# Kernel tuning notes

Measured on AMD Instinct MI355X. Metric: run time of the kernel, lower is better.

Reference implementation:

```python
import jax, jax.numpy as jnp
import numpy as np

D_MODEL = 256
D_FFN = 1024
N_HEADS = 8
N_LEVELS = 4
N_POINTS = 4
SPATIAL = np.array([[60, 100], [30, 50], [15, 25], [8, 13]], dtype=np.int32)  # (H, W) per level


def _layer_norm(x, g, b, eps=1e-5):
    mu = jnp.mean(x, axis=-1, keepdims=True)
    var = jnp.mean(jnp.square(x - mu), axis=-1, keepdims=True)
    return (x - mu) * jax.lax.rsqrt(var + eps) * g + b


def _bilinear_sample(v_l, loc, aw, H, W):
    # v_l: (B,H,W,h,hd); loc: (B,Lq,h,p,2) normalized [0,1]; aw: (B,Lq,h,p)
    B = v_l.shape[0]
    h = v_l.shape[3]
    x = loc[..., 0] * W - 0.5  # grid_sample align_corners=False convention
    y = loc[..., 1] * H - 0.5
    x0 = jnp.floor(x)
    y0 = jnp.floor(y)
    lx = x - x0
    ly = y - y0
    x0i = x0.astype(jnp.int32)
    y0i = y0.astype(jnp.int32)
    bi = jnp.arange(B)[:, None, None, None]
    hi = jnp.arange(h)[None, None, :, None]

    def g(xi, yi):
        valid = (xi >= 0) & (xi < W) & (yi >= 0) & (yi < H)
        xc = jnp.clip(xi, 0, W - 1)
        yc = jnp.clip(yi, 0, H - 1)
        return v_l[bi, yc, xc, hi] * valid[..., None].astype(v_l.dtype)  # zero padding

    w00 = (1 - lx) * (1 - ly)
    w01 = lx * (1 - ly)
    w10 = (1 - lx) * ly
    w11 = lx * ly
    samp = (g(x0i, y0i) * w00[..., None] + g(x0i + 1, y0i) * w01[..., None]
            + g(x0i, y0i + 1) * w10[..., None] + g(x0i + 1, y0i + 1) * w11[..., None])
    # weighted sum over sampling points -> (B,Lq,h,hd)
    return jnp.einsum('blhpd,blhp->blhd', samp, aw)


def _msda(q, val, ref, W_value, b_value, W_off, b_off, W_attn, b_attn, W_out, b_out):
    # mmcv MultiScaleDeformableAttention (batch_first, identity=query, eval-mode dropout)
    B, Lq, C = q.shape
    hd = C // N_HEADS
    v = (val @ W_value + b_value).reshape(B, -1, N_HEADS, hd)
    off = (q @ W_off + b_off).reshape(B, Lq, N_HEADS, N_LEVELS, N_POINTS, 2)
    aw = jax.nn.softmax((q @ W_attn + b_attn).reshape(B, Lq, N_HEADS, N_LEVELS * N_POINTS), axis=-1)
    aw = aw.reshape(B, Lq, N_HEADS, N_LEVELS, N_POINTS)
    normalizer = jnp.asarray(SPATIAL[:, ::-1].copy(), dtype=q.dtype)  # (levels, 2) = (W, H)
    loc = ref[:, :, None, :, None, :] + off / normalizer[None, None, None, :, None, :]
    out = jnp.zeros((B, Lq, N_HEADS, hd), q.dtype)
    start = 0
    for lvl in range(N_LEVELS):
        H, W = int(SPATIAL[lvl, 0]), int(SPATIAL[lvl, 1])
        v_l = v[:, start:start + H * W].reshape(B, H, W, N_HEADS, hd)
        start += H * W
        out = out + _bilinear_sample(v_l, loc[:, :, :, lvl], aw[:, :, :, lvl], H, W)
    return q + out.reshape(B, Lq, C) @ W_out + b_out  # identity + output_proj


def setup_inputs() -> dict:
    key = jax.random.key(0)
    ks = jax.random.split(key, 16)
    bs, cams, nq = 1, 6, 6400
    l = int(SPATIAL.prod(axis=1).sum())
    s = 0.02
    inp = {
        'query': jax.random.normal(ks[0], (bs, nq, D_MODEL), jnp.float32),
        'key': jax.random.normal(ks[1], (bs, cams, l, D_MODEL), jnp.float32),
        'value': jax.random.normal(ks[2], (bs, cams, l, D_MODEL), jnp.float32),
        'reference_points_cam': jax.random.uniform(ks[3], (cams, bs, nq, N_LEVELS, 2), jnp.float32),
        'spatial_shapes': jnp.asarray(SPATIAL),
        'level_start_index': jnp.asarray(np.concatenate([[0], np.cumsum(SPATIAL.prod(axis=1))[:-1]]).astype(np.int32)),
        'bev_mask': jax.random.randint(ks[4], (cams, bs, nq, 4), 0, 2).astype(jnp.int32),
        'W_value': jax.random.normal(ks[5], (D_MODEL, D_MODEL), jnp.float32) * s,
        'b_value': jnp.zeros((D_MODEL,), jnp.float32),
        'W_off': jax.random.normal(ks[6], (D_MODEL, N_HEADS * N_LEVELS * N_POINTS * 2), jnp.float32) * s,
        'b_off': jax.random.normal(ks[7], (N_HEADS * N_LEVELS * N_POINTS * 2,), jnp.float32) * s,
        'W_attn': jax.random.normal(ks[8], (D_MODEL, N_HEADS * N_LEVELS * N_POINTS), jnp.float32) * s,
        'b_attn': jnp.zeros((N_HEADS * N_LEVELS * N_POINTS,), jnp.float32),
        'W_out': jax.random.normal(ks[9], (D_MODEL, D_MODEL), jnp.float32) * s,
        'b_out': jnp.zeros((D_MODEL,), jnp.float32),
        'ln1_g': jnp.ones((D_MODEL,), jnp.float32),
        'ln1_b': jnp.zeros((D_MODEL,), jnp.float32),
        'W1': jax.random.normal(ks[10], (D_MODEL, D_FFN), jnp.float32) * s,
        'b1': jnp.zeros((D_FFN,), jnp.float32),
        'W2': jax.random.normal(ks[11], (D_FFN, D_MODEL), jnp.float32) * s,
        'b2': jnp.zeros((D_MODEL,), jnp.float32),
        'ln2_g': jnp.ones((D_MODEL,), jnp.float32),
        'ln2_b': jnp.zeros((D_MODEL,), jnp.float32),
    }
    return inp


def reference(query, key, value, reference_points_cam, spatial_shapes, level_start_index, bev_mask,
              W_value, b_value, W_off, b_off, W_attn, b_attn, W_out, b_out,
              ln1_g, ln1_b, W1, b1, W2, b2, ln2_g, ln2_b):
    bs, nq, C = query.shape
    cams = key.shape[1]
    l = key.shape[2]
    # per-camera query visibility taken from batch element 0 (as in original)
    cam_mask = (bev_mask[:, 0].sum(-1) > 0).astype(query.dtype)  # (cams, nq)
    # rebatch via masking: equivalent to gather-to-padded since attention is per-query
    q_rb = (query[:, None] * cam_mask[None, :, :, None]).reshape(bs * cams, nq, C)
    ref_rb = (jnp.transpose(reference_points_cam, (1, 0, 2, 3, 4))
              * cam_mask[None, :, :, None, None]).reshape(bs * cams, nq, N_LEVELS, 2)
    val = value.reshape(bs * cams, l, C)
    attn = _msda(q_rb, val, ref_rb, W_value, b_value, W_off, b_off, W_attn, b_attn, W_out, b_out)
    attn = attn.reshape(bs, cams, nq, C)
    # scatter-add back (only visible camera contributions)
    slots = jnp.einsum('bknc,kn->bnc', attn, cam_mask)
    # visibility count (full bev_mask, per batch element)
    count = (bev_mask.sum(-1) > 0).astype(query.dtype)  # (cams, bs, nq)
    count = jnp.maximum(count.transpose(1, 2, 0).sum(-1), 1.0)  # (bs, nq)
    slots = slots / count[..., None]
    x = _layer_norm(slots + query, ln1_g, ln1_b)
    ffn = jax.nn.relu(x @ W1 + b1) @ W2 + b2
    return _layer_norm(x + ffn, ln2_g, ln2_b)
```

## Files before the change

kernel.cpp:

```cpp
#include <hip/hip_runtime.h>
#include <math.h>

#define NQ      6400
#define NCAMS   6
#define LTOT    7979
#define DM      256
#define DFFN    1024

typedef __attribute__((ext_vector_type(8))) short bf16x8;
typedef __attribute__((ext_vector_type(4))) float f32x4;
typedef __attribute__((ext_vector_type(2))) float f32x2;

__device__ inline unsigned short f32_to_bf16(float f) {
    unsigned u = __float_as_uint(f);
    unsigned r = u + 0x7FFF + ((u >> 16) & 1);
    return (unsigned short)(r >> 16);
}

__device__ inline unsigned cvt_pk_bf16(float lo, float hi) {
    unsigned r;
    asm("v_cvt_pk_bf16_f32 %0, %1, %2" : "=v"(r) : "v"(lo), "v"(hi));
    return r;
}
__device__ inline unsigned short cvt1_bf16(float x) {
    return (unsigned short)cvt_pk_bf16(x, 0.f);
}

__global__ __launch_bounds__(256) void wt_head_kernel(
    const float* __restrict__ Wv, const float* __restrict__ Woff,
    const float* __restrict__ Wattn, unsigned short* __restrict__ wsT)
{
    int b = blockIdx.x;
    const float* src; int K, N, t0, dstoff;
    if (b < 64)       { src = Wv;    K = 256; N = 256; t0 = 0;   dstoff = 0; }
    else if (b < 128) { src = Woff;  K = 256; N = 256; t0 = 64;  dstoff = 65536; }
    else              { src = Wattn; K = 256; N = 128; t0 = 128; dstoff = 131072; }
    int t = b - t0;
    int ntn = N >> 5;
    int kt = t / ntn, nt = t - kt * ntn;
    __shared__ float tile[32][33];
    int tx = threadIdx.x & 31, ty = threadIdx.x >> 5;
    #pragma unroll
    for (int i = 0; i < 4; ++i)
        tile[ty + i * 8][tx] = src[(size_t)(kt * 32 + ty + i * 8) * N + nt * 32 + tx];
    __syncthreads();
    #pragma unroll
    for (int i = 0; i < 4; ++i) {
        int nn = nt * 32 + ty + i * 8;
        wsT[dstoff + (size_t)nn * K + kt * 32 + tx] = f32_to_bf16(tile[tx][ty + i * 8]);
    }
}

__global__ __launch_bounds__(256) void head_kernel(
    const float* __restrict__ value, const float* __restrict__ query,
    const unsigned short* __restrict__ WvT, const unsigned short* __restrict__ WqT,
    const float* __restrict__ bv, const float* __restrict__ boff,
    const float* __restrict__ battn,
    unsigned char* __restrict__ vb, unsigned short* __restrict__ qoffb,
    unsigned short* __restrict__ qawb)
{
    __shared__ __align__(16) unsigned char smem[20480];
    const int b = blockIdx.x;
    const int tid = threadIdx.x;
    const int wave = tid >> 6, lane = tid & 63;
    const int wm = wave >> 1, wn = wave & 1;
    const int quad = lane >> 4, l16 = lane & 15;

    if (b < 750) {
        unsigned short (*As)[40] = (unsigned short(*)[40])smem;
        unsigned short (*Bs)[40] = (unsigned short(*)[40])(smem + 10240);
        const int m0 = (b >> 1) * 128, n0 = (b & 1) * 128;
        const int M = NCAMS * LTOT;

        f32x4 acc[4][4] = {};

        for (int k0 = 0; k0 < 256; k0 += 32) {
            #pragma unroll
            for (int i = 0; i < 2; ++i) {
                int idx = tid + 256 * i;
                int r = idx >> 2, kc = (idx & 3) * 8;
                int gr = m0 + r;
                float4 f0, f1;
                if (gr < M) {
                    f0 = *(const float4*)(value + (size_t)gr * 256 + k0 + kc);
                    f1 = *(const float4*)(value + (size_t)gr * 256 + k0 + kc + 4);
                } else { f0 = make_float4(0.f,0.f,0.f,0.f); f1 = f0; }
                uint4 o;
                o.x = cvt_pk_bf16(f0.x, f0.y);
                o.y = cvt_pk_bf16(f0.z, f0.w);
                o.z = cvt_pk_bf16(f1.x, f1.y);
                o.w = cvt_pk_bf16(f1.z, f1.w);
                *(uint4*)&As[r][kc] = o;
            }
            #pragma unroll
            for (int i = 0; i < 2; ++i) {
                int idx = tid + 256 * i;
                int r = idx >> 2, kc = (idx & 3) * 8;
                *(uint4*)&Bs[r][kc] = *(const uint4*)(WvT + (size_t)(n0 + r) * 256 + k0 + kc);
            }
            __syncthreads();
            bf16x8 af[4], bfr[4];
            #pragma unroll
            for (int mi = 0; mi < 4; ++mi)
                af[mi] = *(const bf16x8*)&As[wm * 64 + mi * 16 + l16][quad * 8];
            #pragma unroll
            for (int ni = 0; ni < 4; ++ni)
                bfr[ni] = *(const bf16x8*)&Bs[wn * 64 + ni * 16 + l16][quad * 8];
            #pragma unroll
            for (int mi = 0; mi < 4; ++mi)
                #pragma unroll
                for (int ni = 0; ni < 4; ++ni)
                    acc[mi][ni] = __builtin_amdgcn_mfma_f32_16x16x32_bf16(
                        af[mi], bfr[ni], acc[mi][ni], 0, 0, 0);
            __syncthreads();
        }

        #pragma unroll
        for (int mi = 0; mi < 4; ++mi) {
            #pragma unroll
            for (int r = 0; r < 4; ++r) {
                int gm = m0 + wm * 64 + mi * 16 + quad * 4 + r;
                if (gm >= M) continue;
                int cam = gm / LTOT;
                int pix = gm - cam * LTOT;
                #pragma unroll
                for (int p = 0; p < 2; ++p) {
                    int gn0 = n0 + wn * 64 + p * 32 + l16;
                    int head = gn0 >> 5;
                    float v0 = acc[mi][2 * p][r]     + bv[gn0];
                    float v1 = acc[mi][2 * p + 1][r] + bv[gn0 + 16];
                    int pk = __builtin_amdgcn_cvt_pk_fp8_f32(v0, v1, 0, false);
                    *(unsigned short*)(vb + (((size_t)(cam * 8 + head)) * LTOT + pix) * 32
                                       + 2 * l16) = (unsigned short)pk;
                }
            }
        }
    } else {
        unsigned short (*As)[40] = (unsigned short(*)[40])smem;
        unsigned short (*Bs)[40] = (unsigned short(*)[40])(smem + 5120);
        const int t = b - 750;
        const int bx = t / 100, by = t % 100;
        const int m0 = by * 64, n0 = bx * 128;
        const int is_attn = (bx == 2);

        f32x4 acc[2][4] = {};

        for (int k0 = 0; k0 < 256; k0 += 32) {
            {
                int r = tid >> 2, kc = (tid & 3) * 8;
                float4 f0 = *(const float4*)(query + (size_t)(m0 + r) * 256 + k0 + kc);
                float4 f1 = *(const float4*)(query + (size_t)(m0 + r) * 256 + k0 + kc + 4);
                uint4 o;
                o.x = cvt_pk_bf16(f0.x, f0.y);
                o.y = cvt_pk_bf16(f0.z, f0.w);
                o.z = cvt_pk_bf16(f1.x, f1.y);
                o.w = cvt_pk_bf16(f1.z, f1.w);
                *(uint4*)&As[r][kc] = o;
            }
            #pragma unroll
            for (int i = 0; i < 2; ++i) {
                int idx = tid + 256 * i;
                int r = idx >> 2, kc = (idx & 3) * 8;
                *(uint4*)&Bs[r][kc] = *(const uint4*)(WqT + (size_t)(n0 + r) * 256 + k0 + kc);
            }
            __syncthreads();
            bf16x8 af[2], bfr[4];
            #pragma unroll
            for (int mi = 0; mi < 2; ++mi)
                af[mi] = *(const bf16x8*)&As[wm * 32 + mi * 16 + l16][quad * 8];
            #pragma unroll
            for (int ni = 0; ni < 4; ++ni)
                bfr[ni] = *(const bf16x8*)&Bs[wn * 64 + ni * 16 + l16][quad * 8];
            #pragma unroll
            for (int mi = 0; mi < 2; ++mi)
                #pragma unroll
                for (int ni = 0; ni < 4; ++ni)
                    acc[mi][ni] = __builtin_amdgcn_mfma_f32_16x16x32_bf16(
                        af[mi], bfr[ni], acc[mi][ni], 0, 0, 0);
            __syncthreads();
        }

        if (is_attn) {
            #pragma unroll
            for (int mi = 0; mi < 2; ++mi) {
                #pragma unroll
                for (int r = 0; r < 4; ++r) {
                    int gm = m0 + wm * 32 + mi * 16 + quad * 4 + r;
                    #pragma unroll
                    for (int ni = 0; ni < 4; ++ni) {
                        int gn = wn * 64 + ni * 16 + l16;
                        float v = acc[mi][ni][r] + battn[gn];
                        float mx = v;
                        #pragma unroll
                        for (int s = 1; s < 16; s <<= 1)
                            mx = fmaxf(mx, __shfl_xor(mx, s, 64));
                        float e = __expf(v - mx);
                        float sum = e;
                        #pragma unroll
                        for (int s = 1; s < 16; s <<= 1)
                            sum += __shfl_xor(sum, s, 64);
                        qawb[(size_t)gm * 128 + gn] = f32_to_bf16(e / sum);
                    }
                }
            }
        } else {
            #pragma unroll
            for (int mi = 0; mi < 2; ++mi) {
                #pragma unroll
                for (int r = 0; r < 4; ++r) {
                    int gm = m0 + wm * 32 + mi * 16 + quad * 4 + r;
                    #pragma unroll
                    for (int ni = 0; ni < 4; ++ni) {
                        int gn = n0 + wn * 64 + ni * 16 + l16;
                        qoffb[(size_t)gm * 256 + gn] = f32_to_bf16(acc[mi][ni][r] + boff[gn]);
                    }
                }
            }
        }
    }
}

__global__ __launch_bounds__(256) void sample_kernel(
    const unsigned char* __restrict__ vb,
    const unsigned short* __restrict__ qoffb,
    const unsigned short* __restrict__ qawb,
    const float* __restrict__ refpts,
    const int*   __restrict__ bev_mask,
    const float* __restrict__ Wout, const float* __restrict__ W1,
    const float* __restrict__ W2,
    unsigned short* __restrict__ outsum,
    float* __restrict__ visb,
    unsigned short* __restrict__ wsT)
{
    __shared__ __align__(16) unsigned s_tab[NCAMS][272][4];
    __shared__ float s_vis[NCAMS][16];
    __shared__ int   s_nvis[16];

    const int bid = blockIdx.x;
    const int tid = threadIdx.x;

    if (bid >= 3200) {
        int t = bid - 3200;
        const float* src; int K, N, dstoff;
        if (t < 64)       { src = Wout; K = 256;  N = 256;  dstoff = 163840; }
        else if (t < 320) { src = W1;   K = 256;  N = 1024; dstoff = 229376; t -= 64; }
        else              { src = W2;   K = 1024; N = 256;  dstoff = 491520; t -= 320; }
        int ntn = N >> 5;
        int kt = t / ntn, nt = t - kt * ntn;
        float (*tile)[33] = (float(*)[33])&s_tab[0][0][0];
        int tx = tid & 31, ty = tid >> 5;
        #pragma unroll
        for (int i = 0; i < 4; ++i)
            tile[ty + i * 8][tx] = src[(size_t)(kt * 32 + ty + i * 8) * N + nt * 32 + tx];
        __syncthreads();
        int txp = (dstoff == 163840) ? (((tx & 15) << 1) | (tx >> 4)) : tx;
        #pragma unroll
        for (int i = 0; i < 4; ++i) {
            int nn = nt * 32 + ty + i * 8;
            wsT[dstoff + (size_t)nn * K + kt * 32 + txp] = f32_to_bf16(tile[tx][ty + i * 8]);
        }
        return;
    }

    const int h   = bid & 7;
    const int q0  = (bid >> 3) * 16;
    const int sq  = tid >> 4;
    const int tup = tid & 15;
    const int lvl = tup >> 2;
    const int n_s = q0 + sq;

    if (tid < 96) {
        int cam = tid >> 4, q = tid & 15;
        const int* bm = bev_mask + ((size_t)cam * NQ + q0 + q) * 4;
        s_vis[cam][q] = ((bm[0] + bm[1] + bm[2] + bm[3]) > 0) ? 1.f : 0.f;
    }
    __syncthreads();
    if (tid >= 32 && tid < 48) {
        int q = tid - 32;
        float s = 0.f;
        #pragma unroll
        for (int cam = 0; cam < NCAMS; ++cam) s += s_vis[cam][q];
        s_nvis[q] = (int)s;
    }

    unsigned uoff = *(const unsigned*)(qoffb + (size_t)n_s * 256 + h * 32 + tup * 2);
    const float offx  = __uint_as_float(uoff << 16);
    const float offy  = __uint_as_float(uoff & 0xFFFF0000u);
    const float my_aw = __uint_as_float((unsigned)qawb[(size_t)n_s * 128 + h * 16 + tup] << 16);
    const int Wl   = (lvl == 0) ? 100 : (lvl == 1) ? 50 : (lvl == 2) ? 25 : 13;
    const int Hl   = (lvl == 0) ? 60  : (lvl == 1) ? 30 : (lvl == 2) ? 15 : 8;
    const int base = (lvl == 0) ? 0   : (lvl == 1) ? 6000 : (lvl == 2) ? 7500 : 7875;
    const float dx = offx / (float)Wl;
    const float dy = offy / (float)Hl;
    const int tabi = sq * 17 + tup;

    float2 rp[NCAMS];
    #pragma unroll
    for (int k = 0; k < NCAMS; ++k)
        rp[k] = *(const float2*)(refpts + (((size_t)k * NQ + n_s) * 4 + lvl) * 2);
    __syncthreads();

    #pragma unroll
    for (int k = 0; k < NCAMS; ++k) {
        float fx = (rp[k].x + dx) * (float)Wl - 0.5f;
        float fy = (rp[k].y + dy) * (float)Hl - 0.5f;
        float x0f = floorf(fx), y0f = floorf(fy);
        float lx = fx - x0f, ly = fy - y0f;
        int x0 = (int)x0f, y0 = (int)y0f;
        int x1 = x0 + 1, y1 = y0 + 1;
        float wb = my_aw * s_vis[k][sq];
        float w00 = (1.f - lx) * (1.f - ly) * wb;
        float w01 = lx * (1.f - ly) * wb;
        float w10 = (1.f - lx) * ly * wb;
        float w11 = lx * ly * wb;
        bool vx0 = (x0 >= 0) & (x0 < Wl), vx1 = (x1 >= 0) & (x1 < Wl);
        bool vy0 = (y0 >= 0) & (y0 < Hl), vy1 = (y1 >= 0) & (y1 < Hl);
        uint4 o;
        o.x = (vx0 & vy0) ? (((unsigned)(base + y0 * Wl + x0) << 16) | f32_to_bf16(w00)) : 0u;
        o.y = (vx1 & vy0) ? (((unsigned)(base + y0 * Wl + x1) << 16) | f32_to_bf16(w01)) : 0u;
        o.z = (vx0 & vy1) ? (((unsigned)(base + y1 * Wl + x0) << 16) | f32_to_bf16(w10)) : 0u;
        o.w = (vx1 & vy1) ? (((unsigned)(base + y1 * Wl + x1) << 16) | f32_to_bf16(w11)) : 0u;
        *(uint4*)&s_tab[k][tabi][0] = o;
    }
    __syncthreads();

    const int tp  = (tid >> 1) & 7;
    const int cg2 = tid & 1;

    f32x2 A[8] = {};

    #pragma unroll
    for (int k = 0; k < NCAMS; ++k) {
        const char* vkh = (const char*)vb + (size_t)(k * 8 + h) * (LTOT * 32) + cg2 * 16;
        #pragma unroll
        for (int t = 0; t < 2; ++t) {
            uint4 t4 = *(const uint4*)&s_tab[k][sq * 17 + tp * 2 + t][0];
            #pragma unroll
            for (int corner = 0; corner < 4; ++corner) {
                unsigned tc = (corner == 0) ? t4.x : (corner == 1) ? t4.y
                            : (corner == 2) ? t4.z : t4.w;
                float w = __uint_as_float(tc << 16);
                f32x2 w2 = {w, w};
                uint4 d = *(const uint4*)(vkh + ((size_t)(tc >> 16) << 5));
                A[0] += w2 * __builtin_amdgcn_cvt_pk_f32_fp8(d.x, false);
                A[1] += w2 * __builtin_amdgcn_cvt_pk_f32_fp8(d.x, true);
                A[2] += w2 * __builtin_amdgcn_cvt_pk_f32_fp8(d.y, false);
                A[3] += w2 * __builtin_amdgcn_cvt_pk_f32_fp8(d.y, true);
                A[4] += w2 * __builtin_amdgcn_cvt_pk_f32_fp8(d.z, false);
                A[5] += w2 * __builtin_amdgcn_cvt_pk_f32_fp8(d.z, true);
                A[6] += w2 * __builtin_amdgcn_cvt_pk_f32_fp8(d.w, false);
                A[7] += w2 * __builtin_amdgcn_cvt_pk_f32_fp8(d.w, true);
            }
        }
    }

    #pragma unroll
    for (int i = 0; i < 8; ++i) {
        float x0 = A[i].x, x1 = A[i].y;
        x0 += __shfl_xor(x0, 2, 64); x1 += __shfl_xor(x1, 2, 64);
        x0 += __shfl_xor(x0, 4, 64); x1 += __shfl_xor(x1, 4, 64);
        x0 += __shfl_xor(x0, 8, 64); x1 += __shfl_xor(x1, 8, 64);
        A[i].x = x0; A[i].y = x1;
    }

    if ((tid & 14) == 0) {
        int nv = s_nvis[sq];
        float sc = 1.f / (float)(nv > 0 ? nv : 1);
        uint4 o0, o1;
        o0.x = f32_to_bf16(A[0].x * sc) | ((unsigned)f32_to_bf16(A[0].y * sc) << 16);
        o0.y = f32_to_bf16(A[1].x * sc) | ((unsigned)f32_to_bf16(A[1].y * sc) << 16);
        o0.z = f32_to_bf16(A[2].x * sc) | ((unsigned)f32_to_bf16(A[2].y * sc) << 16);
        o0.w = f32_to_bf16(A[3].x * sc) | ((unsigned)f32_to_bf16(A[3].y * sc) << 16);
        o1.x = f32_to_bf16(A[4].x * sc) | ((unsigned)f32_to_bf16(A[4].y * sc) << 16);
        o1.y = f32_to_bf16(A[5].x * sc) | ((unsigned)f32_to_bf16(A[5].y * sc) << 16);
        o1.z = f32_to_bf16(A[6].x * sc) | ((unsigned)f32_to_bf16(A[6].y * sc) << 16);
        o1.w = f32_to_bf16(A[7].x * sc) | ((unsigned)f32_to_bf16(A[7].y * sc) << 16);
        *(uint4*)(outsum + (size_t)n_s * 256 + h * 32 + cg2 * 16)     = o0;
        *(uint4*)(outsum + (size_t)n_s * 256 + h * 32 + cg2 * 16 + 8) = o1;
    }
    if (h == 0 && tid < 16) visb[q0 + tid] = (s_nvis[tid] > 0) ? 1.f : 0.f;
}

__global__ __launch_bounds__(256) void tail_kernel(
    const unsigned short* __restrict__ A,
    const unsigned short* __restrict__ BT,
    const unsigned short* __restrict__ W1T,
    const unsigned short* __restrict__ W2T,
    const float* __restrict__ query, const float* __restrict__ visb,
    const float* __restrict__ b_out,
    const float* __restrict__ g1, const float* __restrict__ bln1,
    const float* __restrict__ fb1, const float* __restrict__ fb2,
    const float* __restrict__ g2, const float* __restrict__ bln2,
    float* __restrict__ out)
{
    __shared__ __align__(16) unsigned short As[32][40];
    __shared__ __align__(16) unsigned short Bs[256][40];
    __shared__ __align__(16) unsigned short Bs2[128][72];
    __shared__ __align__(16) unsigned short xs[32][264];
    __shared__ __align__(16) unsigned short hs[32][136];
    __shared__ float sred[2][4][4][2];
    __shared__ float ssred[2][4][4][2];
    __shared__ float s_mu[32], s_rs[32];

    const int tid  = threadIdx.x;
    const int wave = tid >> 6, lane = tid & 63;
    const int wm = wave >> 1, wn = wave & 1;
    const int quad = lane >> 4, l16 = lane & 15;
    const int m0 = blockIdx.x * 32;

    f32x4 acc[8] = {};

    for (int k0 = 0; k0 < 256; k0 += 32) {
        {
            int r = tid >> 3, kc = (tid & 7) * 4;
            *(uint2*)&As[r][kc] = *(const uint2*)(A + (size_t)(m0 + r) * 256 + k0 + kc);
        }
        {
            const unsigned short* src = BT + (size_t)tid * 256 + k0;
            *(uint4*)&Bs[tid][0]  = *(const uint4*)(src);
            *(uint4*)&Bs[tid][8]  = *(const uint4*)(src + 8);
            *(uint4*)&Bs[tid][16] = *(const uint4*)(src + 16);
            *(uint4*)&Bs[tid][24] = *(const uint4*)(src + 24);
        }
        __syncthreads();
        bf16x8 af = *(const bf16x8*)&As[wm * 16 + l16][quad * 8];
        #pragma unroll
        for (int ni = 0; ni < 8; ++ni) {
            bf16x8 bfr = *(const bf16x8*)&Bs[wn * 128 + ni * 16 + l16][quad * 8];
            acc[ni] = __builtin_amdgcn_mfma_f32_16x16x32_bf16(af, bfr, acc[ni], 0, 0, 0);
        }
        __syncthreads();
    }

    float vals[8][4];
    #pragma unroll
    for (int r = 0; r < 4; ++r) {
        int gm = m0 + wm * 16 + quad * 4 + r;
        float vs = visb[gm];
        float s = 0.f, ss = 0.f;
        #pragma unroll
        for (int ni = 0; ni < 8; ++ni) {
            int gn = wn * 128 + ni * 16 + l16;
            float v = acc[ni][r] + vs * b_out[gn]
                    + query[(size_t)gm * 256 + gn] * (1.f + vs);
            vals[ni][r] = v;
            s += v; ss += v * v;
        }
        #pragma unroll
        for (int m = 1; m < 16; m <<= 1) {
            s  += __shfl_xor(s,  m, 64);
            ss += __shfl_xor(ss, m, 64);
        }
        if (l16 == 0) {
            sred[wm][quad][r][wn]  = s;
            ssred[wm][quad][r][wn] = ss;
        }
    }
    __syncthreads();
    if (tid < 32) {
        int lwm = tid >> 4, lq = (tid >> 2) & 3, lr = tid & 3;
        float s  = sred[lwm][lq][lr][0]  + sred[lwm][lq][lr][1];
        float ss = ssred[lwm][lq][lr][0] + ssred[lwm][lq][lr][1];
        float mu = s * (1.f / 256.f);
        float var = ss * (1.f / 256.f) - mu * mu;
        s_mu[tid] = mu;
        s_rs[tid] = rsqrtf(var + 1e-5f);
    }
    __syncthreads();

    #pragma unroll
    for (int r = 0; r < 4; ++r) {
        int rowl = wm * 16 + quad * 4 + r;
        float mu = s_mu[rowl], rs = s_rs[rowl];
        #pragma unroll
        for (int ni = 0; ni < 8; ++ni) {
            int gn = wn * 128 + ni * 16 + l16;
            float res = (vals[ni][r] - mu) * rs * g1[gn] + bln1[gn];
            vals[ni][r] = res;
            xs[rowl][gn] = cvt1_bf16(res);
        }
    }

    f32x4 acc2[8] = {};

    for (int nc = 0; nc < 8; ++nc) {
        f32x4 hacc[4] = {};
        for (int k0 = 0; k0 < 256; k0 += 64) {
            #pragma unroll
            for (int i = 0; i < 4; ++i) {
                int idx = tid + 256 * i;
                int rr = idx >> 3, c8 = (idx & 7) * 8;
                *(uint4*)&Bs2[rr][c8] =
                    *(const uint4*)(W1T + (size_t)(nc * 128 + rr) * 256 + k0 + c8);
            }
            __syncthreads();
            #pragma unroll
            for (int s = 0; s < 2; ++s) {
                bf16x8 a2 = *(const bf16x8*)&xs[wm * 16 + l16][k0 + s * 32 + quad * 8];
                #pragma unroll
                for (int ni = 0; ni < 4; ++ni) {
                    bf16x8 b2v = *(const bf16x8*)&Bs2[wn * 64 + ni * 16 + l16][s * 32 + quad * 8];
                    hacc[ni] = __builtin_amdgcn_mfma_f32_16x16x32_bf16(a2, b2v, hacc[ni], 0, 0, 0);
                }
            }
            __syncthreads();
        }
        #pragma unroll
        for (int ni = 0; ni < 4; ++ni) {
            #pragma unroll
            for (int r = 0; r < 4; ++r) {
                int rowl = wm * 16 + quad * 4 + r;
                int col  = wn * 64 + ni * 16 + l16;
                hs[rowl][col] = cvt1_bf16(fmaxf(hacc[ni][r] + fb1[nc * 128 + col], 0.f));
            }
        }
        __syncthreads();
        #pragma unroll
        for (int ks = 0; ks < 4; ++ks) {
            {
                const unsigned short* src = W2T + (size_t)tid * 1024 + nc * 128 + ks * 32;
                *(uint4*)&Bs[tid][0]  = *(const uint4*)(src);
                *(uint4*)&Bs[tid][8]  = *(const uint4*)(src + 8);
                *(uint4*)&Bs[tid][16] = *(const uint4*)(src + 16);
                *(uint4*)&Bs[tid][24] = *(const uint4*)(src + 24);
            }
            __syncthreads();
            bf16x8 a3 = *(const bf16x8*)&hs[wm * 16 + l16][ks * 32 + quad * 8];
            #pragma unroll
            for (int ni = 0; ni < 8; ++ni) {
                bf16x8 b3 = *(const bf16x8*)&Bs[wn * 128 + ni * 16 + l16][quad * 8];
                acc2[ni] = __builtin_amdgcn_mfma_f32_16x16x32_bf16(a3, b3, acc2[ni], 0, 0, 0);
            }
            __syncthreads();
        }
    }

    #pragma unroll
    for (int r = 0; r < 4; ++r) {
        float s = 0.f, ss = 0.f;
        #pragma unroll
        for (int ni = 0; ni < 8; ++ni) {
            int gn = wn * 128 + ni * 16 + l16;
            float t = vals[ni][r] + acc2[ni][r] + fb2[gn];
            vals[ni][r] = t;
            s += t; ss += t * t;
        }
        #pragma unroll
        for (int m = 1; m < 16; m <<= 1) {
            s  += __shfl_xor(s,  m, 64);
            ss += __shfl_xor(ss, m, 64);
        }
        if (l16 == 0) {
            sred[wm][quad][r][wn]  = s;
            ssred[wm][quad][r][wn] = ss;
        }
    }
    __syncthreads();
    if (tid < 32) {
        int lwm = tid >> 4, lq = (tid >> 2) & 3, lr = tid & 3;
        float s  = sred[lwm][lq][lr][0]  + sred[lwm][lq][lr][1];
        float ss = ssred[lwm][lq][lr][0] + ssred[lwm][lq][lr][1];
        float mu = s * (1.f / 256.f);
        float var = ss * (1.f / 256.f) - mu * mu;
        s_mu[tid] = mu;
        s_rs[tid] = rsqrtf(var + 1e-5f);
    }
    __syncthreads();

    #pragma unroll
    for (int r = 0; r < 4; ++r) {
        int rowl = wm * 16 + quad * 4 + r;
        int gm = m0 + rowl;
        float mu = s_mu[rowl], rs = s_rs[rowl];
        #pragma unroll
        for (int ni = 0; ni < 8; ++ni) {
            int gn = wn * 128 + ni * 16 + l16;
            out[(size_t)gm * 256 + gn] = (vals[ni][r] - mu) * rs * g2[gn] + bln2[gn];
        }
    }
}

extern "C" void kernel_launch(void* const* d_in, const int* in_sizes, int n_in,
                              void* d_out, int out_size, void* d_ws, size_t ws_size,
                              hipStream_t stream)
{
    const float* query   = (const float*)d_in[0];
    const float* value   = (const float*)d_in[2];
    const float* refpts  = (const float*)d_in[3];
    const int*   bevmask = (const int*)d_in[6];
    const float* W_value = (const float*)d_in[7];
    const float* b_value = (const float*)d_in[8];
    const float* W_off   = (const float*)d_in[9];
    const float* b_off   = (const float*)d_in[10];
    const float* W_attn  = (const float*)d_in[11];
    const float* b_attn  = (const float*)d_in[12];
    const float* W_out   = (const float*)d_in[13];
    const float* b_out   = (const float*)d_in[14];
    const float* ln1_g   = (const float*)d_in[15];
    const float* ln1_b   = (const float*)d_in[16];
    const float* W1      = (const float*)d_in[17];
    const float* b1      = (const float*)d_in[18];
    const float* W2      = (const float*)d_in[19];
    const float* b2      = (const float*)d_in[20];
    const float* ln2_g   = (const float*)d_in[21];
    const float* ln2_b   = (const float*)d_in[22];
    float* out = (float*)d_out;

    char* ws = (char*)d_ws;
    unsigned char*  vb     = (unsigned char*)(ws + 0);
    unsigned short* qoffb  = (unsigned short*)(ws + 27000000);
    unsigned short* qawb   = (unsigned short*)(ws + 31000000);
    unsigned short* outsum = (unsigned short*)(ws + 33000000);
    float*          visb   = (float*)(ws + 36500000);
    unsigned short* wsT    = (unsigned short*)(ws + 36600000);

    unsigned short* WvT = wsT;
    unsigned short* WqT = wsT + 65536;
    unsigned short* WoT = wsT + 163840;
    unsigned short* W1T = wsT + 229376;
    unsigned short* W2T = wsT + 491520;

    wt_head_kernel<<<dim3(160), 256, 0, stream>>>(
        W_value, W_off, W_attn, wsT);
    head_kernel<<<dim3(1050), 256, 0, stream>>>(
        value, query, WvT, WqT, b_value, b_off, b_attn, vb, qoffb, qawb);
    sample_kernel<<<dim3(3776), 256, 0, stream>>>(
        vb, qoffb, qawb, refpts, bevmask, W_out, W1, W2, outsum, visb, wsT);
    tail_kernel<<<dim3(200), 256, 0, stream>>>(
        outsum, WoT, W1T, W2T, query, visb, b_out,
        ln1_g, ln1_b, b1, b2, ln2_g, ln2_b, out);
}
```

Measured before the change: 285.3 us.

## Load GEMM operand fragments directly from global memory in tail kernel

Removes the shared-memory staging of A, W_out^T, W1^T and W2^T tiles in the fused output-projection/LN/FFN tail kernel. Each wave now reads its MFMA operand fragments straight from global memory (weights are L2-resident), which drops most __syncthreads barriers and frees LDS. It also sets launch_bounds to (256,1) and fully unrolls the K loops. The trade-off is redundant global/L2 reads, since the two waves sharing a row block each fetch their own B fragments, and less coalesced 16-byte per-lane accesses. Register pressure may also rise with the occupancy hint.

```diff
diff --git a/kernel.cpp b/kernel.cpp
--- a/kernel.cpp
+++ b/kernel.cpp
@@ -381,7 +381,7 @@
     if (h == 0 && tid < 16) visb[q0 + tid] = (s_nvis[tid] > 0) ? 1.f : 0.f;
 }
 
-__global__ __launch_bounds__(256) void tail_kernel(
+__global__ __launch_bounds__(256, 1) void tail_kernel(
     const unsigned short* __restrict__ A,
     const unsigned short* __restrict__ BT,
     const unsigned short* __restrict__ W1T,
@@ -393,9 +393,6 @@
     const float* __restrict__ g2, const float* __restrict__ bln2,
     float* __restrict__ out)
 {
-    __shared__ __align__(16) unsigned short As[32][40];
-    __shared__ __align__(16) unsigned short Bs[256][40];
-    __shared__ __align__(16) unsigned short Bs2[128][72];
     __shared__ __align__(16) unsigned short xs[32][264];
     __shared__ __align__(16) unsigned short hs[32][136];
     __shared__ float sred[2][4][4][2];
@@ -407,29 +404,18 @@
     const int wm = wave >> 1, wn = wave & 1;
     const int quad = lane >> 4, l16 = lane & 15;
     const int m0 = blockIdx.x * 32;
+    const int arow = wm * 16 + l16;
 
     f32x4 acc[8] = {};
-
+    #pragma unroll
     for (int k0 = 0; k0 < 256; k0 += 32) {
-        {
-            int r = tid >> 3, kc = (tid & 7) * 4;
-            *(uint2*)&As[r][kc] = *(const uint2*)(A + (size_t)(m0 + r) * 256 + k0 + kc);
-        }
-        {
-            const unsigned short* src = BT + (size_t)tid * 256 + k0;
-            *(uint4*)&Bs[tid][0]  = *(const uint4*)(src);
-            *(uint4*)&Bs[tid][8]  = *(const uint4*)(src + 8);
-            *(uint4*)&Bs[tid][16] = *(const uint4*)(src + 16);
-            *(uint4*)&Bs[tid][24] = *(const uint4*)(src + 24);
-        }
-        __syncthreads();
-        bf16x8 af = *(const bf16x8*)&As[wm * 16 + l16][quad * 8];
+        bf16x8 af = *(const bf16x8*)(A + (size_t)(m0 + arow) * 256 + k0 + quad * 8);
         #pragma unroll
         for (int ni = 0; ni < 8; ++ni) {
-            bf16x8 bfr = *(const bf16x8*)&Bs[wn * 128 + ni * 16 + l16][quad * 8];
+            bf16x8 bfr = *(const bf16x8*)(BT + (size_t)(wn * 128 + ni * 16 + l16) * 256
+                                          + k0 + quad * 8);
             acc[ni] = __builtin_amdgcn_mfma_f32_16x16x32_bf16(af, bfr, acc[ni], 0, 0, 0);
         }
-        __syncthreads();
     }
 
     float vals[8][4];
@@ -480,31 +466,23 @@
             xs[rowl][gn] = cvt1_bf16(res);
         }
     }
+    __syncthreads();
 
     f32x4 acc2[8] = {};
 
     for (int nc = 0; nc < 8; ++nc) {
         f32x4 hacc[4] = {};
-        for (int k0 = 0; k0 < 256; k0 += 64) {
-            #pragma unroll
-            for (int i = 0; i < 4; ++i) {
-                int idx = tid + 256 * i;
-                int rr = idx >> 3, c8 = (idx & 7) * 8;
-                *(uint4*)&Bs2[rr][c8] =
-                    *(const uint4*)(W1T + (size_t)(nc * 128 + rr) * 256 + k0 + c8);
-            }
-            __syncthreads();
-            #pragma unroll
-            for (int s = 0; s < 2; ++s) {
-                bf16x8 a2 = *(const bf16x8*)&xs[wm * 16 + l16][k0 + s * 32 + quad * 8];
-                #pragma unroll
-                for (int ni = 0; ni < 4; ++ni) {
-                    bf16x8 b2v = *(const bf16x8*)&Bs2[wn * 64 + ni * 16 + l16][s * 32 + quad * 8];
-                    hacc[ni] = __builtin_amdgcn_mfma_f32_16x16x32_bf16(a2, b2v, hacc[ni], 0, 0, 0);
-                }
-            }
-            __syncthreads();
-        }
+        #pragma unroll
+        for (int k0 = 0; k0 < 256; k0 += 32) {
+            bf16x8 a2 = *(const bf16x8*)&xs[arow][k0 + quad * 8];
+            #pragma unroll
+            for (int ni = 0; ni < 4; ++ni) {
+                bf16x8 b2v = *(const bf16x8*)(W1T
+                    + (size_t)(nc * 128 + wn * 64 + ni * 16 + l16) * 256 + k0 + quad * 8);
+                hacc[ni] = __builtin_amdgcn_mfma_f32_16x16x32_bf16(a2, b2v, hacc[ni], 0, 0, 0);
+            }
+        }
+        __syncthreads();
         #pragma unroll
         for (int ni = 0; ni < 4; ++ni) {
             #pragma unroll
@@ -517,21 +495,13 @@
         __syncthreads();
         #pragma unroll
         for (int ks = 0; ks < 4; ++ks) {
-            {
-                const unsigned short* src = W2T + (size_t)tid * 1024 + nc * 128 + ks * 32;
-                *(uint4*)&Bs[tid][0]  = *(const uint4*)(src);
-                *(uint4*)&Bs[tid][8]  = *(const uint4*)(src + 8);
-                *(uint4*)&Bs[tid][16] = *(const uint4*)(src + 16);
-                *(uint4*)&Bs[tid][24] = *(const uint4*)(src + 24);
-            }
-            __syncthreads();
-            bf16x8 a3 = *(const bf16x8*)&hs[wm * 16 + l16][ks * 32 + quad * 8];
+            bf16x8 a3 = *(const bf16x8*)&hs[arow][ks * 32 + quad * 8];
             #pragma unroll
             for (int ni = 0; ni < 8; ++ni) {
-                bf16x8 b3 = *(const bf16x8*)&Bs[wn * 128 + ni * 16 + l16][quad * 8];
+                bf16x8 b3 = *(const bf16x8*)(W2T
+                    + (size_t)(wn * 128 + ni * 16 + l16) * 1024 + nc * 128 + ks * 32 + quad * 8);
                 acc2[ni] = __builtin_amdgcn_mfma_f32_16x16x32_bf16(a3, b3, acc2[ni], 0, 0, 0);
             }
-            __syncthreads();
         }
     }
 
```

Result: slower. 297.6 us (+4.3%).
